# Kernel optimization log

Hardware: AMD Instinct MI355X
Metric: run time of the kernel (lower is better)

## Reference

```python
import jax, jax.numpy as jnp
import numpy as np

N = 65536        # nodes
E = 1048576      # edges (avg degree 16)
G = 512          # graphs
D_IN = 128       # input_dim
D1 = 128         # latent_dim1
D2 = 128         # latent_dim2
L = 3            # layer_num
B = 2            # blocks_num
K = 10           # K_cluster
NF = 16          # num_graph_filter
C = 10           # n_classes
EPS = 1e-5


def setup_inputs():
    key = jax.random.key(0)
    ks = jax.random.split(key, 20)
    s = 0.05
    return {
        "features": jax.random.normal(ks[0], (N, D_IN), jnp.float32),
        "W_row": jax.random.randint(ks[1], (E,), 0, N, jnp.int32),
        "W_col": jax.random.randint(ks[2], (E,), 0, N, jnp.int32),
        "W_vals": jax.random.uniform(ks[3], (E,), jnp.float32),
        "graph_indicator": jnp.sort(jax.random.randint(ks[4], (N,), 0, G, jnp.int32)),
        "targets": jax.random.randint(ks[5], (G,), 0, C, jnp.int32),
        "enc_w1": jax.random.normal(ks[6], (B, D_IN, 2 * D2)) * s,
        "enc_b1": jnp.zeros((B, 2 * D2)),
        "enc_w2": jax.random.normal(ks[7], (B, 2 * D2, D1)) * s,
        "enc_b2": jnp.zeros((B, D1)),
        "bn_gamma": jnp.ones((L + 1, D1)),
        "bn_beta": jnp.zeros((L + 1, D1)),
        "concat_w1": jax.random.normal(ks[8], (L + 1, D2)) * s,
        "concat_b1": jnp.zeros((D2,)),
        "concat_w2": jax.random.normal(ks[9], (D2, 1)) * s,
        "concat_b2": jnp.zeros((1,)),
        "smlp_w1": jax.random.normal(ks[10], (D1, D2)) * s,
        "smlp_b1": jnp.zeros((D2,)),
        "smlp_w2": jax.random.normal(ks[11], (D2, K)) * s,
        "smlp_b2": jnp.zeros((K,)),
        "proto_w1": jax.random.normal(ks[12], (D1, D1)) * s,
        "proto_b1": jnp.zeros((D1,)),
        "proto_w2": jax.random.normal(ks[13], (D1, NF)) * s,
        "proto_b2": jnp.zeros((NF,)),
        "final_w": jax.random.normal(ks[14], (D1 * K, C)) * s,
        "final_b": jnp.zeros((C,)),
        "corr_inter": jax.random.uniform(ks[15], (C, NF)),
        "corr_intra": jax.random.uniform(ks[16], (C, NF)),
    }


def _bn(x, g, b):
    # training-mode batch norm over the node axis (axis=-2), biased variance
    m = x.mean(axis=-2, keepdims=True)
    v = x.var(axis=-2, keepdims=True)
    return (x - m) / jnp.sqrt(v + EPS) * g + b


def reference(features, W_row, W_col, W_vals, graph_indicator, targets,
              enc_w1, enc_b1, enc_w2, enc_b2, bn_gamma, bn_beta,
              concat_w1, concat_b1, concat_w2, concat_b2,
              smlp_w1, smlp_b1, smlp_w2, smlp_b2,
              proto_w1, proto_b1, proto_w2, proto_b2,
              final_w, final_b, corr_inter, corr_intra):
    def spmm(X):  # W @ X via edge list, [N, D] -> [N, D]
        return jax.ops.segment_sum(W_vals[:, None] * X[W_col], W_row, num_segments=N)

    # block encoders -> [B, N, D1]
    h = jax.nn.relu(jnp.einsum('nd,bdh->bnh', features, enc_w1) + enc_b1[:, None, :])
    X_blocks = jnp.einsum('bnh,bho->bno', h, enc_w2) + enc_b2[:, None, :]

    hidden_rep = [X_blocks.mean(0)]
    prop = X_blocks  # holds W^p @ X_b (recursive equivalent of W_list[p] @ X_b)
    for p in range(L):
        prop = jnp.stack([spmm(prop[b]) for b in range(B)])
        Hb = jax.nn.relu(_bn(prop, bn_gamma[p], bn_beta[p]))  # BN per block call, shared params
        hidden_rep.append(Hb.mean(0))

    # concat_mlp acts elementwise per (node, channel) across the layer axis
    Hst = jnp.stack(hidden_rep, axis=-1)  # [N, D1, L+1]
    hc = jax.nn.relu(jnp.einsum('ndl,lh->ndh', Hst, concat_w1) + concat_b1)
    H_all = jnp.einsum('ndh,h->nd', hc, concat_w2[:, 0]) + concat_b2[0]
    H_all = jax.nn.relu(_bn(H_all, bn_gamma[L], bn_beta[L]))

    S_all = jax.nn.softmax(jax.nn.relu(H_all @ smlp_w1 + smlp_b1) @ smlp_w2 + smlp_b2, axis=1)

    # per-graph cluster pooling E_g = S_g^T @ H_g, vectorized via segment_sum
    E_all = jax.ops.segment_sum(S_all[:, :, None] * H_all[:, None, :], graph_indicator, num_segments=G)  # [G, K, D1]

    pred1 = E_all.reshape(G, -1) @ final_w + final_b
    pred_softmax = jax.nn.softmax(pred1, axis=-1)

    sample_cat = jax.random.categorical(jax.random.key(42), pred1, axis=-1)
    ind_positive_sample = sample_cat == targets
    oh = jax.nn.one_hot(sample_cat, C)
    epsilon = jax.lax.stop_gradient(jnp.where(oh != 0, 1.0 - pred_softmax, -pred_softmax))
    sample_cat_oh = pred_softmax + epsilon  # straight-through one-hot

    Q = jax.nn.softmax(jax.nn.relu(E_all @ proto_w1 + proto_b1) @ proto_w2 + proto_b2, axis=-1)  # [G, K, NF]
    corr = jax.nn.softmax(corr_inter, axis=0) * jax.nn.softmax(corr_intra, axis=1)  # [C, NF]
    corr_mask = sample_cat_oh @ corr  # [G, NF]
    feature_mask = jnp.sum(Q * corr_mask[:, None, :], axis=-1)  # [G, K]
    pred2 = (feature_mask[:, :, None] * E_all).reshape(G, -1) @ final_w + final_b

    return pred1, pred2, S_all, H_all, ind_positive_sample, E_all, Q
```

## Files before the change

kernel.cpp:

```cpp
#include <hip/hip_runtime.h>
#include <math.h>

#define NN 65536
#define EE 1048576
#define GG 512
#define D  128

typedef float4 f4;

__global__ __launch_bounds__(256) void k_gemm(const float* __restrict__ A,
    const float* __restrict__ B, const float* __restrict__ bias,
    float* __restrict__ C, int M, int N, int K, int relu)
{
    __shared__ __align__(16) float As[16][132];
    __shared__ __align__(16) float Bs[16][132];
    int tid = threadIdx.x;
    int tx = tid & 15, ty = tid >> 4;
    int row0 = blockIdx.y * 128, col0 = blockIdx.x * 128;
    float acc[8][8];
#pragma unroll
    for (int i = 0; i < 8; ++i)
#pragma unroll
        for (int j = 0; j < 8; ++j) acc[i][j] = 0.f;
    int ar = tid >> 1, ac = (tid & 1) * 8;
    int br = tid >> 4, bc = (tid & 15) * 8;
    const float* aptr = A + (size_t)(row0 + ar) * K + ac;
    const float* bptr = B + (size_t)br * N + col0 + bc;

    f4 pa0 = *(const f4*)(aptr);
    f4 pa1 = *(const f4*)(aptr + 4);
    f4 pb0 = *(const f4*)(bptr);
    f4 pb1 = *(const f4*)(bptr + 4);

    for (int k0 = 0; k0 < K; k0 += 16) {
        As[ac + 0][ar] = pa0.x; As[ac + 1][ar] = pa0.y; As[ac + 2][ar] = pa0.z; As[ac + 3][ar] = pa0.w;
        As[ac + 4][ar] = pa1.x; As[ac + 5][ar] = pa1.y; As[ac + 6][ar] = pa1.z; As[ac + 7][ar] = pa1.w;
        *(f4*)&Bs[br][bc] = pb0; *(f4*)&Bs[br][bc + 4] = pb1;
        __syncthreads();
        if (k0 + 16 < K) {
            pa0 = *(const f4*)(aptr + k0 + 16);
            pa1 = *(const f4*)(aptr + k0 + 16 + 4);
            pb0 = *(const f4*)(bptr + (size_t)(k0 + 16) * N);
            pb1 = *(const f4*)(bptr + (size_t)(k0 + 16) * N + 4);
        }
#pragma unroll
        for (int kk = 0; kk < 16; ++kk) {
            float a[8], b[8];
            *(f4*)&a[0] = *(const f4*)&As[kk][ty * 4];
            *(f4*)&a[4] = *(const f4*)&As[kk][64 + ty * 4];
            *(f4*)&b[0] = *(const f4*)&Bs[kk][tx * 4];
            *(f4*)&b[4] = *(const f4*)&Bs[kk][64 + tx * 4];
#pragma unroll
            for (int i = 0; i < 8; ++i)
#pragma unroll
                for (int j = 0; j < 8; ++j) acc[i][j] = fmaf(a[i], b[j], acc[i][j]);
        }
        __syncthreads();
    }
    f4 bia0 = *(const f4*)(bias + col0 + tx * 4);
    f4 bia1 = *(const f4*)(bias + col0 + 64 + tx * 4);
#pragma unroll
    for (int i = 0; i < 8; ++i) {
        int r = row0 + ((i < 4) ? (ty * 4 + i) : (64 + ty * 4 + i - 4));
        f4 v0, v1;
#pragma unroll
        for (int j = 0; j < 4; ++j) {
            float u0 = acc[i][j] + (&bia0.x)[j];
            float u1 = acc[i][j + 4] + (&bia1.x)[j];
            if (relu) { u0 = fmaxf(u0, 0.f); u1 = fmaxf(u1, 0.f); }
            (&v0.x)[j] = u0; (&v1.x)[j] = u1;
        }
        *(f4*)(C + (size_t)r * N + col0 + tx * 4) = v0;
        *(f4*)(C + (size_t)r * N + col0 + 64 + tx * 4) = v1;
    }
}

__global__ __launch_bounds__(256) void k_hist(const int* __restrict__ Wr, int* __restrict__ cnt)
{
    int e = blockIdx.x * 256 + threadIdx.x;
    if (e < EE) atomicAdd(&cnt[Wr[e]], 1);
}

__global__ __launch_bounds__(256) void k_scan1(const int* __restrict__ cnt,
    int* __restrict__ excl, int* __restrict__ bsum)
{
    __shared__ int s[256];
    int b = blockIdx.x, t = threadIdx.x;
    int v = cnt[b * 256 + t];
    s[t] = v; __syncthreads();
    for (int o = 1; o < 256; o <<= 1) {
        int x = (t >= o) ? s[t - o] : 0;
        __syncthreads();
        s[t] += x;
        __syncthreads();
    }
    excl[b * 256 + t] = s[t] - v;
    if (t == 255) bsum[b] = s[255];
}

__global__ void k_scan2(const int* __restrict__ bsum, int* __restrict__ boff)
{
    __shared__ int s[256];
    int t = threadIdx.x;
    int v = bsum[t]; s[t] = v; __syncthreads();
    for (int o = 1; o < 256; o <<= 1) {
        int x = (t >= o) ? s[t - o] : 0;
        __syncthreads();
        s[t] += x;
        __syncthreads();
    }
    boff[t] = s[t] - v;
}

__global__ __launch_bounds__(256) void k_scan3(const int* __restrict__ excl, const int* __restrict__ boff,
    int* __restrict__ rowptr, int* __restrict__ cursor)
{
    int i = blockIdx.x * 256 + threadIdx.x;
    int v = excl[i] + boff[i >> 8];
    rowptr[i] = v; cursor[i] = v;
    if (i == 0) rowptr[NN] = EE;
}

__global__ __launch_bounds__(256) void k_scatter(const int* __restrict__ Wr, const int* __restrict__ Wc,
    const float* __restrict__ Wv, int* __restrict__ cursor, int* __restrict__ ecol, float* __restrict__ ev)
{
    int e = blockIdx.x * 256 + threadIdx.x;
    if (e >= EE) return;
    int r = Wr[e];
    int p = atomicAdd(&cursor[r], 1);
    ecol[p] = Wc[e]; ev[p] = Wv[e];
}

__global__ __launch_bounds__(256) void k_spmm(const int* __restrict__ rowptr,
    const int* __restrict__ ecol, const float* __restrict__ eval,
    const float* __restrict__ X, float* __restrict__ Y)
{
    int row = blockIdx.x * 4 + (threadIdx.x >> 6);
    int lane = threadIdx.x & 63;
    int s = rowptr[row], e = rowptr[row + 1];
    float a0 = 0.f, a1 = 0.f;
    int i = s;
    for (; i + 4 <= e; i += 4) {
        int   c0 = ecol[i], c1 = ecol[i + 1], c2 = ecol[i + 2], c3 = ecol[i + 3];
        float w0 = eval[i], w1 = eval[i + 1], w2 = eval[i + 2], w3 = eval[i + 3];
        float2 x0 = *(const float2*)(X + (size_t)c0 * D + lane * 2);
        float2 x1 = *(const float2*)(X + (size_t)c1 * D + lane * 2);
        float2 x2 = *(const float2*)(X + (size_t)c2 * D + lane * 2);
        float2 x3 = *(const float2*)(X + (size_t)c3 * D + lane * 2);
        a0 = fmaf(w0, x0.x, a0); a1 = fmaf(w0, x0.y, a1);
        a0 = fmaf(w1, x1.x, a0); a1 = fmaf(w1, x1.y, a1);
        a0 = fmaf(w2, x2.x, a0); a1 = fmaf(w2, x2.y, a1);
        a0 = fmaf(w3, x3.x, a0); a1 = fmaf(w3, x3.y, a1);
    }
    for (; i < e; ++i) {
        int cc = ecol[i];
        float w = eval[i];
        float2 x = *(const float2*)(X + (size_t)cc * D + lane * 2);
        a0 = fmaf(w, x.x, a0);
        a1 = fmaf(w, x.y, a1);
    }
    *(float2*)(Y + (size_t)row * D + lane * 2) = make_float2(a0, a1);
}

__global__ __launch_bounds__(128) void k_bnstats2(const float* __restrict__ X0, const float* __restrict__ X1,
    double* __restrict__ psum, double* __restrict__ pssq)
{
    const float* __restrict__ X = blockIdx.y ? X1 : X0;
    int d = threadIdx.x;
    int r0 = blockIdx.x * 128;
    double s = 0.0, q = 0.0;
#pragma unroll 4
    for (int r = r0; r < r0 + 128; ++r) {
        double v = (double)X[(size_t)r * D + d];
        s += v; q = fma(v, v, q);
    }
    psum[blockIdx.y * 65536 + blockIdx.x * 128 + d] = s;
    pssq[blockIdx.y * 65536 + blockIdx.x * 128 + d] = q;
}

__global__ void k_bnfin(const double* __restrict__ psum, const double* __restrict__ pssq,
    const float* __restrict__ gamma, const float* __restrict__ beta,
    double* __restrict__ a, double* __restrict__ c, int nb, int layer)
{
    int t = threadIdx.x;
    if (t >= nb * 128) return;
    int blk = t >> 7, d = t & 127;
    const double* ps = psum + blk * 65536;
    const double* pq = pssq + blk * 65536;
    double s = 0.0, q = 0.0;
    for (int j = 0; j < 512; ++j) { s += ps[j * 128 + d]; q += pq[j * 128 + d]; }
    double m = s * (1.0 / 65536.0);
    double v = q * (1.0 / 65536.0) - m * m;
    double aa = (double)gamma[layer * 128 + d] / sqrt(v + 1e-5);
    a[t] = aa;
    c[t] = (double)beta[layer * 128 + d] - m * aa;
}

__global__ __launch_bounds__(256) void k_mean2(const f4* __restrict__ x0, const f4* __restrict__ x1,
                                               f4* __restrict__ o)
{
    int i = blockIdx.x * 256 + threadIdx.x;
    f4 a = x0[i], b = x1[i];
    f4 r;
    r.x = 0.5f * (a.x + b.x); r.y = 0.5f * (a.y + b.y);
    r.z = 0.5f * (a.z + b.z); r.w = 0.5f * (a.w + b.w);
    o[i] = r;
}

__global__ __launch_bounds__(256) void k_hidden(const f4* __restrict__ p0, const f4* __restrict__ p1,
    const double* __restrict__ a, const double* __restrict__ c, f4* __restrict__ o)
{
    int i = blockIdx.x * 256 + threadIdx.x;
    int d4 = (i & 31) * 4;
    f4 x = p0[i], y = p1[i];
    f4 r;
#pragma unroll
    for (int j = 0; j < 4; ++j) {
        float a0 = (float)a[d4 + j], c0 = (float)c[d4 + j];
        float a1 = (float)a[128 + d4 + j], c1 = (float)c[128 + d4 + j];
        float xv = (&x.x)[j], yv = (&y.x)[j];
        (&r.x)[j] = 0.5f * (fmaxf(fmaf(xv, a0, c0), 0.f) + fmaxf(fmaf(yv, a1, c1), 0.f));
    }
    o[i] = r;
}

__global__ __launch_bounds__(256) void k_bnapply(f4* __restrict__ H,
    const double* __restrict__ a, const double* __restrict__ c)
{
    int i = blockIdx.x * 256 + threadIdx.x;
    int d4 = (i & 31) * 4;
    f4 x = H[i];
#pragma unroll
    for (int j = 0; j < 4; ++j) {
        float a0 = (float)a[d4 + j], c0 = (float)c[d4 + j];
        (&x.x)[j] = fmaxf(fmaf((&x.x)[j], a0, c0), 0.f);
    }
    H[i] = x;
}

__global__ __launch_bounds__(256) void k_concat(const f4* __restrict__ h0, const f4* __restrict__ h1,
    const f4* __restrict__ h2, const f4* __restrict__ h3,
    const float* __restrict__ w1, const float* __restrict__ b1,
    const float* __restrict__ w2, const float* __restrict__ b2,
    f4* __restrict__ Hpre)
{
    __shared__ __align__(16) float sw0[128], sw1_[128], sw2_[128], sw3[128], sv[128], sb[128];
    int t = threadIdx.x;
    if (t < 128) {
        sw0[t] = w1[t];        sw1_[t] = w1[128 + t];
        sw2_[t] = w1[256 + t]; sw3[t]  = w1[384 + t];
        sv[t]  = w2[t];        sb[t]   = b1[t];
    }
    __syncthreads();
    int i = blockIdx.x * 256 + t;
    f4 x0 = h0[i], x1 = h1[i], x2 = h2[i], x3 = h3[i];
    float bb2 = b2[0];
    float acc0 = bb2, acc1 = bb2, acc2 = bb2, acc3 = bb2;
    for (int h4 = 0; h4 < D; h4 += 4) {
        f4 cw0 = *(const f4*)&sw0[h4];
        f4 cw1 = *(const f4*)&sw1_[h4];
        f4 cw2 = *(const f4*)&sw2_[h4];
        f4 cw3 = *(const f4*)&sw3[h4];
        f4 cbb = *(const f4*)&sb[h4];
        f4 cvv = *(const f4*)&sv[h4];
#pragma unroll
        for (int j = 0; j < 4; ++j) {
            float w0 = (&cw0.x)[j], ww1 = (&cw1.x)[j], ww2 = (&cw2.x)[j], w3 = (&cw3.x)[j];
            float bb = (&cbb.x)[j], vv = (&cvv.x)[j];
            float t0 = fmaf(x3.x, w3, fmaf(x2.x, ww2, fmaf(x1.x, ww1, fmaf(x0.x, w0, bb))));
            float t1 = fmaf(x3.y, w3, fmaf(x2.y, ww2, fmaf(x1.y, ww1, fmaf(x0.y, w0, bb))));
            float t2 = fmaf(x3.z, w3, fmaf(x2.z, ww2, fmaf(x1.z, ww1, fmaf(x0.z, w0, bb))));
            float t3 = fmaf(x3.w, w3, fmaf(x2.w, ww2, fmaf(x1.w, ww1, fmaf(x0.w, w0, bb))));
            acc0 = fmaf(fmaxf(t0, 0.f), vv, acc0);
            acc1 = fmaf(fmaxf(t1, 0.f), vv, acc1);
            acc2 = fmaf(fmaxf(t2, 0.f), vv, acc2);
            acc3 = fmaf(fmaxf(t3, 0.f), vv, acc3);
        }
    }
    f4 r; r.x = acc0; r.y = acc1; r.z = acc2; r.w = acc3;
    Hpre[i] = r;
}

__global__ __launch_bounds__(256) void k_s(const float* __restrict__ hid,
    const float* __restrict__ w2, const float* __restrict__ b2, float* __restrict__ S)
{
    int n = blockIdx.x * 256 + threadIdx.x;
    if (n >= NN) return;
    const float* hr = hid + (size_t)n * D;
    float s[10];
#pragma unroll
    for (int k = 0; k < 10; ++k) s[k] = b2[k];
    for (int h = 0; h < D; h += 4) {
        f4 hv = *(const f4*)(hr + h);
#pragma unroll
        for (int k = 0; k < 10; ++k) {
            s[k] = fmaf(hv.x, w2[(h + 0) * 10 + k], s[k]);
            s[k] = fmaf(hv.y, w2[(h + 1) * 10 + k], s[k]);
            s[k] = fmaf(hv.z, w2[(h + 2) * 10 + k], s[k]);
            s[k] = fmaf(hv.w, w2[(h + 3) * 10 + k], s[k]);
        }
    }
    float m = s[0];
#pragma unroll
    for (int k = 1; k < 10; ++k) m = fmaxf(m, s[k]);
    float e[10], sum = 0.f;
#pragma unroll
    for (int k = 0; k < 10; ++k) { e[k] = expf(s[k] - m); sum += e[k]; }
    float inv = 1.f / sum;
#pragma unroll
    for (int k = 0; k < 10; ++k) S[(size_t)n * 10 + k] = e[k] * inv;
}

__global__ __launch_bounds__(256) void k_eall(const float* __restrict__ S, const float* __restrict__ H,
    const int* __restrict__ off, float* __restrict__ Eo, double* __restrict__ E64)
{
    int g = blockIdx.x;
    int d = threadIdx.x & 127;
    int half = threadIdx.x >> 7;
    double acc[5] = {0.0, 0.0, 0.0, 0.0, 0.0};
    int s0 = off[g], s1 = off[g + 1];
    for (int n = s0; n < s1; ++n) {
        double hv = (double)H[(size_t)n * D + d];
#pragma unroll
        for (int j = 0; j < 5; ++j) acc[j] = fma((double)S[(size_t)n * 10 + half * 5 + j], hv, acc[j]);
    }
#pragma unroll
    for (int j = 0; j < 5; ++j) {
        size_t o = (size_t)g * 1280 + (half * 5 + j) * D + d;
        Eo[o] = (float)acc[j];
        E64[o] = acc[j];
    }
}

__global__ void k_off(const int* __restrict__ gi, int* __restrict__ off)
{
    int g = blockIdx.x * 256 + threadIdx.x;
    if (g > GG) return;
    int lo = 0, hi = NN;
    while (lo < hi) { int mid = (lo + hi) >> 1; if (gi[mid] < g) lo = mid + 1; else hi = mid; }
    off[g] = lo;
}

__global__ void k_corr(const float* __restrict__ ci, const float* __restrict__ ca, float* __restrict__ corr)
{
    int t = threadIdx.x;
    if (t >= 160) return;
    int r = t / 16, c = t % 16;
    double m = -1e300;
    for (int i = 0; i < 10; ++i) m = fmax(m, (double)ci[i * 16 + c]);
    double s = 0.0;
    for (int i = 0; i < 10; ++i) s += exp((double)ci[i * 16 + c] - m);
    double vi = exp((double)ci[r * 16 + c] - m) / s;
    double m2 = -1e300;
    for (int j = 0; j < 16; ++j) m2 = fmax(m2, (double)ca[r * 16 + j]);
    double s2 = 0.0;
    for (int j = 0; j < 16; ++j) s2 += exp((double)ca[r * 16 + j] - m2);
    double va = exp((double)ca[r * 16 + c] - m2) / s2;
    corr[t] = (float)(vi * va);
}

__device__ __forceinline__ unsigned tf_rotl(unsigned x, unsigned n) { return (x << n) | (x >> (32u - n)); }

__global__ void k_gumbel(double* __restrict__ out)
{
    int i = blockIdx.x * 256 + threadIdx.x;
    if (i >= 5120) return;
    unsigned x0 = 0u;
    unsigned x1 = (unsigned)i;
    const unsigned ks0 = 0u, ks1 = 42u;
    const unsigned ks2 = 0x1BD11BDAu ^ ks0 ^ ks1;
    x0 += ks0; x1 += ks1;
#define TF_ROUND(rr) { x0 += x1; x1 = tf_rotl(x1, rr); x1 ^= x0; }
    TF_ROUND(13) TF_ROUND(15) TF_ROUND(26) TF_ROUND(6)
    x0 += ks1; x1 += ks2 + 1u;
    TF_ROUND(17) TF_ROUND(29) TF_ROUND(16) TF_ROUND(24)
    x0 += ks2; x1 += ks0 + 2u;
    TF_ROUND(13) TF_ROUND(15) TF_ROUND(26) TF_ROUND(6)
    x0 += ks0; x1 += ks1 + 3u;
    TF_ROUND(17) TF_ROUND(29) TF_ROUND(16) TF_ROUND(24)
    x0 += ks1; x1 += ks2 + 4u;
    TF_ROUND(13) TF_ROUND(15) TF_ROUND(26) TF_ROUND(6)
    x0 += ks2; x1 += ks0 + 5u;
#undef TF_ROUND
    unsigned bits = x0 ^ x1;
    unsigned fb = (bits >> 9) | 0x3f800000u;
    float f = __uint_as_float(fb) - 1.0f;
    const float tinyf = 1.1754943508222875e-38f;
    float u32v = fmaxf(tinyf, f * (1.0f - tinyf) + tinyf);
    out[i] = -log(-log((double)u32v));
}

__global__ __launch_bounds__(64) void k_pred1(const double* __restrict__ E64, const float* __restrict__ fw,
    const float* __restrict__ fb, const double* __restrict__ gum, const int* __restrict__ tgt,
    const float* __restrict__ corr, float* __restrict__ pred1, float* __restrict__ ind,
    float* __restrict__ cmask)
{
    int g = blockIdx.x;
    int l = threadIdx.x;
    double acc[10];
#pragma unroll
    for (int c = 0; c < 10; ++c) acc[c] = 0.0;
    for (int i = l; i < 1280; i += 64) {
        double e = E64[(size_t)g * 1280 + i];
#pragma unroll
        for (int c = 0; c < 10; ++c) acc[c] = fma(e, (double)fw[i * 10 + c], acc[c]);
    }
#pragma unroll
    for (int c = 0; c < 10; ++c) {
        double v = acc[c];
        for (int o = 32; o > 0; o >>= 1) v += __shfl_down(v, o, 64);
        acc[c] = v;
    }
    if (l == 0) {
        double best = -1e300; int bi = 0;
        for (int c = 0; c < 10; ++c) {
            double p = acc[c] + (double)fb[c];
            pred1[g * 10 + c] = (float)p;
            double y = p + gum[g * 10 + c];
            if (y > best) { best = y; bi = c; }
        }
        ind[g] = (bi == tgt[g]) ? 1.f : 0.f;
        for (int f = 0; f < 16; ++f) cmask[g * 16 + f] = corr[bi * 16 + f];
    }
}

__global__ __launch_bounds__(128) void k_q(const float* __restrict__ Eo, const float* __restrict__ w1,
    const float* __restrict__ b1, const float* __restrict__ w2, const float* __restrict__ b2,
    const float* __restrict__ cmask, float* __restrict__ Q, float* __restrict__ fm)
{
    int gk = blockIdx.x;
    int g = gk / 10;
    int h = threadIdx.x;
    __shared__ float e[128];
    __shared__ float hh[128];
    __shared__ float qv[16];
    __shared__ float pr[16];
    e[h] = Eo[(size_t)gk * D + h];
    __syncthreads();
    float acc = b1[h];
#pragma unroll 8
    for (int d = 0; d < D; ++d) acc = fmaf(e[d], w1[d * D + h], acc);
    hh[h] = fmaxf(acc, 0.f);
    __syncthreads();
    if (h < 16) {
        float s = b2[h];
        for (int d = 0; d < D; ++d) s = fmaf(hh[d], w2[d * 16 + h], s);
        qv[h] = s;
    }
    __syncthreads();
    if (h < 16) {
        float m = qv[0];
        for (int f = 1; f < 16; ++f) m = fmaxf(m, qv[f]);
        pr[h] = expf(qv[h] - m);
    }
    __syncthreads();
    if (h < 16) {
        float s = 0.f;
        for (int f = 0; f < 16; ++f) s += pr[f];
        float q = pr[h] / s;
        Q[(size_t)gk * 16 + h] = q;
        qv[h] = q * cmask[g * 16 + h];
    }
    __syncthreads();
    if (h == 0) {
        float s = 0.f;
        for (int f = 0; f < 16; ++f) s += qv[f];
        fm[gk] = s;
    }
}

__global__ __launch_bounds__(64) void k_pred2(const double* __restrict__ E64, const float* __restrict__ fw,
    const float* __restrict__ fb, const float* __restrict__ fm, float* __restrict__ pred2)
{
    int g = blockIdx.x;
    int l = threadIdx.x;
    double acc[10];
#pragma unroll
    for (int c = 0; c < 10; ++c) acc[c] = 0.0;
    for (int i = l; i < 1280; i += 64) {
        int k = i >> 7;
        double e = E64[(size_t)g * 1280 + i] * (double)fm[g * 10 + k];
#pragma unroll
        for (int c = 0; c < 10; ++c) acc[c] = fma(e, (double)fw[i * 10 + c], acc[c]);
    }
#pragma unroll
    for (int c = 0; c < 10; ++c) {
        double v = acc[c];
        for (int o = 32; o > 0; o >>= 1) v += __shfl_down(v, o, 64);
        acc[c] = v;
    }
    if (l == 0)
        for (int c = 0; c < 10; ++c) pred2[g * 10 + c] = (float)(acc[c] + (double)fb[c]);
}

extern "C" void kernel_launch(void* const* d_in, const int* in_sizes, int n_in,
                              void* d_out, int out_size, void* d_ws, size_t ws_size,
                              hipStream_t stream)
{
    const float* features = (const float*)d_in[0];
    const int*   W_row    = (const int*)d_in[1];
    const int*   W_col    = (const int*)d_in[2];
    const float* W_vals   = (const float*)d_in[3];
    const int*   gi       = (const int*)d_in[4];
    const int*   targets  = (const int*)d_in[5];
    const float* enc_w1   = (const float*)d_in[6];
    const float* enc_b1   = (const float*)d_in[7];
    const float* enc_w2   = (const float*)d_in[8];
    const float* enc_b2   = (const float*)d_in[9];
    const float* bn_gamma = (const float*)d_in[10];
    const float* bn_beta  = (const float*)d_in[11];
    const float* concat_w1= (const float*)d_in[12];
    const float* concat_b1= (const float*)d_in[13];
    const float* concat_w2= (const float*)d_in[14];
    const float* concat_b2= (const float*)d_in[15];
    const float* smlp_w1  = (const float*)d_in[16];
    const float* smlp_b1  = (const float*)d_in[17];
    const float* smlp_w2  = (const float*)d_in[18];
    const float* smlp_b2  = (const float*)d_in[19];
    const float* proto_w1 = (const float*)d_in[20];
    const float* proto_b1 = (const float*)d_in[21];
    const float* proto_w2 = (const float*)d_in[22];
    const float* proto_b2 = (const float*)d_in[23];
    const float* final_w  = (const float*)d_in[24];
    const float* final_b  = (const float*)d_in[25];
    const float* corr_i   = (const float*)d_in[26];
    const float* corr_a   = (const float*)d_in[27];

    float* out = (float*)d_out;
    float* o_pred1 = out + 0;
    float* o_pred2 = out + 5120;
    float* o_S     = out + 10240;
    float* o_H     = out + 665600;
    float* o_ind   = out + 9054208;
    float* o_E     = out + 9054720;
    float* o_Q     = out + 9710080;

    char* base = (char*)d_ws;
    size_t off = 0;
    auto alloc = [&](size_t n) -> char* {
        char* r = base + off;
        off = (off + n + 255) & ~(size_t)255;
        return r;
    };
    int*    d_off   = (int*)alloc(513 * 4);
    double* d_a     = (double*)alloc(256 * 8);
    double* d_c     = (double*)alloc(256 * 8);
    double* d_gum   = (double*)alloc(5120 * 8);
    float*  d_corr  = (float*)alloc(160 * 4);
    float*  d_cmask = (float*)alloc(512 * 16 * 4);
    float*  d_fm    = (float*)alloc(5120 * 4);
    double* psum    = (double*)alloc(2 * 512 * 128 * 8);
    double* pssq    = (double*)alloc(2 * 512 * 128 * 8);
    int*    cnt     = (int*)alloc((size_t)NN * 4);
    int*    excl    = (int*)alloc((size_t)NN * 4);
    int*    bsum    = (int*)alloc(256 * 4);
    int*    boff    = (int*)alloc(256 * 4);
    int*    rowptr  = (int*)alloc((size_t)(NN + 1) * 4);
    int*    cursor  = (int*)alloc((size_t)NN * 4);
    int*    ecol    = (int*)alloc((size_t)EE * 4);
    float*  evalv   = (float*)alloc((size_t)EE * 4);
    double* E64     = (double*)alloc((size_t)GG * 1280 * 8);

    const size_t SZ = (size_t)NN * D * 4;
    float* rot0 = (float*)alloc(SZ);
    float* rot1 = (float*)alloc(SZ);
    float* rot2 = (float*)alloc(SZ);
    float* h0   = (float*)alloc(SZ);
    float* h1   = (float*)alloc(SZ);
    float* h2   = (float*)alloc(SZ);
    float* h3   = (float*)alloc(SZ);
    float* Tenc = h0;
    float* hid2 = rot0;

    k_off   <<<3, 256, 0, stream>>>(gi, d_off);
    k_corr  <<<1, 256, 0, stream>>>(corr_i, corr_a, d_corr);
    k_gumbel<<<20, 256, 0, stream>>>(d_gum);

    hipMemsetAsync(cnt, 0, (size_t)NN * 4, stream);
    k_hist   <<<EE / 256, 256, 0, stream>>>(W_row, cnt);
    k_scan1  <<<256, 256, 0, stream>>>(cnt, excl, bsum);
    k_scan2  <<<1, 256, 0, stream>>>(bsum, boff);
    k_scan3  <<<256, 256, 0, stream>>>(excl, boff, rowptr, cursor);
    k_scatter<<<EE / 256, 256, 0, stream>>>(W_row, W_col, W_vals, cursor, ecol, evalv);

    k_gemm<<<dim3(2, 512), 256, 0, stream>>>(features, enc_w1,             enc_b1,       Tenc, NN, 256, 128, 1);
    k_gemm<<<dim3(1, 512), 256, 0, stream>>>(Tenc,     enc_w2,             enc_b2,       rot0, NN, 128, 256, 0);
    k_gemm<<<dim3(2, 512), 256, 0, stream>>>(features, enc_w1 + 128 * 256, enc_b1 + 256, Tenc, NN, 256, 128, 1);
    k_gemm<<<dim3(1, 512), 256, 0, stream>>>(Tenc,     enc_w2 + 256 * 128, enc_b2 + 128, rot1, NN, 128, 256, 0);
    k_mean2<<<8192, 256, 0, stream>>>((const f4*)rot0, (const f4*)rot1, (f4*)h0);

    float* cur0 = rot0;
    float* cur1 = rot1;
    float* fre  = rot2;
    float* hbuf[4] = { h0, h1, h2, h3 };
    for (int p = 0; p < 3; ++p) {
        k_spmm<<<NN / 4, 256, 0, stream>>>(rowptr, ecol, evalv, cur0, fre);
        k_spmm<<<NN / 4, 256, 0, stream>>>(rowptr, ecol, evalv, cur1, cur0);
        k_bnstats2<<<dim3(512, 2), 128, 0, stream>>>(fre, cur0, psum, pssq);
        k_bnfin<<<1, 256, 0, stream>>>(psum, pssq, bn_gamma, bn_beta, d_a, d_c, 2, p);
        k_hidden<<<8192, 256, 0, stream>>>((const f4*)fre, (const f4*)cur0, d_a, d_c, (f4*)hbuf[1 + p]);
        float* t0 = fre; float* t1 = cur0; float* t2 = cur1;
        cur0 = t0; cur1 = t1; fre = t2;
    }

    k_concat<<<8192, 256, 0, stream>>>((const f4*)h0, (const f4*)h1, (const f4*)h2, (const f4*)h3,
                                       concat_w1, concat_b1, concat_w2, concat_b2, (f4*)o_H);
    k_bnstats2<<<dim3(512, 1), 128, 0, stream>>>(o_H, o_H, psum, pssq);
    k_bnfin<<<1, 256, 0, stream>>>(psum, pssq, bn_gamma, bn_beta, d_a, d_c, 1, 3);
    k_bnapply<<<8192, 256, 0, stream>>>((f4*)o_H, d_a, d_c);

    k_gemm<<<dim3(1, 512), 256, 0, stream>>>(o_H, smlp_w1, smlp_b1, hid2, NN, 128, 128, 1);
    k_s<<<256, 256, 0, stream>>>(hid2, smlp_w2, smlp_b2, o_S);

    k_eall <<<512, 256, 0, stream>>>(o_S, o_H, d_off, o_E, E64);
    k_pred1<<<512, 64, 0, stream>>>(E64, final_w, final_b, d_gum, targets, d_corr,
                                    o_pred1, o_ind, d_cmask);
    k_q    <<<5120, 128, 0, stream>>>(o_E, proto_w1, proto_b1, proto_w2, proto_b2,
                                      d_cmask, o_Q, d_fm);
    k_pred2<<<512, 64, 0, stream>>>(E64, final_w, final_b, d_fm, o_pred2);

    (void)in_sizes; (void)n_in; (void)out_size; (void)ws_size;
}
```

Before: 1.325 ms.

## Double-buffer GEMM smem, fuse mean into GEMM epilogue, batch paired SpMMs

The GEMM kernel now double-buffers its shared-memory tiles, so it needs one barrier per k-step instead of two. The epilogue of the last encoder GEMM can also write the average with a second buffer, which removes the separate mean kernel and one full read/write pass. The two SpMM launches per layer are merged into one launch with a 2D grid, and buffers are reassigned so the branches are not overwritten. The cost is double the shared memory per GEMM block, which may reduce occupancy, plus more complex buffer aliasing.

```diff
diff --git a/kernel.cpp b/kernel.cpp
--- a/kernel.cpp
+++ b/kernel.cpp
@@ -10,10 +10,11 @@
 
 __global__ __launch_bounds__(256) void k_gemm(const float* __restrict__ A,
     const float* __restrict__ B, const float* __restrict__ bias,
-    float* __restrict__ C, int M, int N, int K, int relu)
-{
-    __shared__ __align__(16) float As[16][132];
-    __shared__ __align__(16) float Bs[16][132];
+    float* __restrict__ C, const float* __restrict__ mix_src, float* __restrict__ mix_dst,
+    int M, int N, int K, int relu)
+{
+    __shared__ __align__(16) float As[2][16][132];
+    __shared__ __align__(16) float Bs[2][16][132];
     int tid = threadIdx.x;
     int tx = tid & 15, ty = tid >> 4;
     int row0 = blockIdx.y * 128, col0 = blockIdx.x * 128;
@@ -31,32 +32,44 @@
     f4 pa1 = *(const f4*)(aptr + 4);
     f4 pb0 = *(const f4*)(bptr);
     f4 pb1 = *(const f4*)(bptr + 4);
-
+    As[0][ac + 0][ar] = pa0.x; As[0][ac + 1][ar] = pa0.y; As[0][ac + 2][ar] = pa0.z; As[0][ac + 3][ar] = pa0.w;
+    As[0][ac + 4][ar] = pa1.x; As[0][ac + 5][ar] = pa1.y; As[0][ac + 6][ar] = pa1.z; As[0][ac + 7][ar] = pa1.w;
+    *(f4*)&Bs[0][br][bc] = pb0; *(f4*)&Bs[0][br][bc + 4] = pb1;
+    __syncthreads();
+
+    int cur = 0;
     for (int k0 = 0; k0 < K; k0 += 16) {
-        As[ac + 0][ar] = pa0.x; As[ac + 1][ar] = pa0.y; As[ac + 2][ar] = pa0.z; As[ac + 3][ar] = pa0.w;
-        As[ac + 4][ar] = pa1.x; As[ac + 5][ar] = pa1.y; As[ac + 6][ar] = pa1.z; As[ac + 7][ar] = pa1.w;
-        *(f4*)&Bs[br][bc] = pb0; *(f4*)&Bs[br][bc + 4] = pb1;
-        __syncthreads();
-        if (k0 + 16 < K) {
+        int last = (k0 + 16 >= K);
+        if (!last) {
             pa0 = *(const f4*)(aptr + k0 + 16);
             pa1 = *(const f4*)(aptr + k0 + 16 + 4);
             pb0 = *(const f4*)(bptr + (size_t)(k0 + 16) * N);
             pb1 = *(const f4*)(bptr + (size_t)(k0 + 16) * N + 4);
         }
+        const float (*Ac)[132] = As[cur];
+        const float (*Bc)[132] = Bs[cur];
 #pragma unroll
         for (int kk = 0; kk < 16; ++kk) {
             float a[8], b[8];
-            *(f4*)&a[0] = *(const f4*)&As[kk][ty * 4];
-            *(f4*)&a[4] = *(const f4*)&As[kk][64 + ty * 4];
-            *(f4*)&b[0] = *(const f4*)&Bs[kk][tx * 4];
-            *(f4*)&b[4] = *(const f4*)&Bs[kk][64 + tx * 4];
+            *(f4*)&a[0] = *(const f4*)&Ac[kk][ty * 4];
+            *(f4*)&a[4] = *(const f4*)&Ac[kk][64 + ty * 4];
+            *(f4*)&b[0] = *(const f4*)&Bc[kk][tx * 4];
+            *(f4*)&b[4] = *(const f4*)&Bc[kk][64 + tx * 4];
 #pragma unroll
             for (int i = 0; i < 8; ++i)
 #pragma unroll
                 for (int j = 0; j < 8; ++j) acc[i][j] = fmaf(a[i], b[j], acc[i][j]);
         }
-        __syncthreads();
-    }
+        if (!last) {
+            int nxt = cur ^ 1;
+            As[nxt][ac + 0][ar] = pa0.x; As[nxt][ac + 1][ar] = pa0.y; As[nxt][ac + 2][ar] = pa0.z; As[nxt][ac + 3][ar] = pa0.w;
+            As[nxt][ac + 4][ar] = pa1.x; As[nxt][ac + 5][ar] = pa1.y; As[nxt][ac + 6][ar] = pa1.z; As[nxt][ac + 7][ar] = pa1.w;
+            *(f4*)&Bs[nxt][br][bc] = pb0; *(f4*)&Bs[nxt][br][bc + 4] = pb1;
+            __syncthreads();
+            cur = nxt;
+        }
+    }
+
     f4 bia0 = *(const f4*)(bias + col0 + tx * 4);
     f4 bia1 = *(const f4*)(bias + col0 + 64 + tx * 4);
 #pragma unroll
@@ -72,6 +85,18 @@
         }
         *(f4*)(C + (size_t)r * N + col0 + tx * 4) = v0;
         *(f4*)(C + (size_t)r * N + col0 + 64 + tx * 4) = v1;
+        if (mix_dst) {
+            f4 m0 = *(const f4*)(mix_src + (size_t)r * N + col0 + tx * 4);
+            f4 m1 = *(const f4*)(mix_src + (size_t)r * N + col0 + 64 + tx * 4);
+            f4 w0, w1;
+#pragma unroll
+            for (int j = 0; j < 4; ++j) {
+                (&w0.x)[j] = 0.5f * ((&v0.x)[j] + (&m0.x)[j]);
+                (&w1.x)[j] = 0.5f * ((&v1.x)[j] + (&m1.x)[j]);
+            }
+            *(f4*)(mix_dst + (size_t)r * N + col0 + tx * 4) = w0;
+            *(f4*)(mix_dst + (size_t)r * N + col0 + 64 + tx * 4) = w1;
+        }
     }
 }
 
@@ -131,12 +156,15 @@
     ecol[p] = Wc[e]; ev[p] = Wv[e];
 }
 
-__global__ __launch_bounds__(256) void k_spmm(const int* __restrict__ rowptr,
+__global__ __launch_bounds__(256) void k_spmm2(const int* __restrict__ rowptr,
     const int* __restrict__ ecol, const float* __restrict__ eval,
-    const float* __restrict__ X, float* __restrict__ Y)
+    const float* __restrict__ X0, float* __restrict__ Y0,
+    const float* __restrict__ X1, float* __restrict__ Y1)
 {
     int row = blockIdx.x * 4 + (threadIdx.x >> 6);
     int lane = threadIdx.x & 63;
+    const float* __restrict__ X = blockIdx.y ? X1 : X0;
+    float* __restrict__ Y = blockIdx.y ? Y1 : Y0;
     int s = rowptr[row], e = rowptr[row + 1];
     float a0 = 0.f, a1 = 0.f;
     int i = s;
@@ -196,19 +224,8 @@
     c[t] = (double)beta[layer * 128 + d] - m * aa;
 }
 
-__global__ __launch_bounds__(256) void k_mean2(const f4* __restrict__ x0, const f4* __restrict__ x1,
-                                               f4* __restrict__ o)
-{
-    int i = blockIdx.x * 256 + threadIdx.x;
-    f4 a = x0[i], b = x1[i];
-    f4 r;
-    r.x = 0.5f * (a.x + b.x); r.y = 0.5f * (a.y + b.y);
-    r.z = 0.5f * (a.z + b.z); r.w = 0.5f * (a.w + b.w);
-    o[i] = r;
-}
-
-__global__ __launch_bounds__(256) void k_hidden(const f4* __restrict__ p0, const f4* __restrict__ p1,
-    const double* __restrict__ a, const double* __restrict__ c, f4* __restrict__ o)
+__global__ __launch_bounds__(256) void k_hidden(const f4* __restrict__ p0, const f4* p1,
+    const double* __restrict__ a, const double* __restrict__ c, f4* o)
 {
     int i = blockIdx.x * 256 + threadIdx.x;
     int d4 = (i & 31) * 4;
@@ -569,7 +586,7 @@
     float* h1   = (float*)alloc(SZ);
     float* h2   = (float*)alloc(SZ);
     float* h3   = (float*)alloc(SZ);
-    float* Tenc = h0;
+    float* Tenc = h2;
     float* hid2 = rot0;
 
     k_off   <<<3, 256, 0, stream>>>(gi, d_off);
@@ -583,24 +600,25 @@
     k_scan3  <<<256, 256, 0, stream>>>(excl, boff, rowptr, cursor);
     k_scatter<<<EE / 256, 256, 0, stream>>>(W_row, W_col, W_vals, cursor, ecol, evalv);
 
-    k_gemm<<<dim3(2, 512), 256, 0, stream>>>(features, enc_w1,             enc_b1,       Tenc, NN, 256, 128, 1);
-    k_gemm<<<dim3(1, 512), 256, 0, stream>>>(Tenc,     enc_w2,             enc_b2,       rot0, NN, 128, 256, 0);
-    k_gemm<<<dim3(2, 512), 256, 0, stream>>>(features, enc_w1 + 128 * 256, enc_b1 + 256, Tenc, NN, 256, 128, 1);
-    k_gemm<<<dim3(1, 512), 256, 0, stream>>>(Tenc,     enc_w2 + 256 * 128, enc_b2 + 128, rot1, NN, 128, 256, 0);
-    k_mean2<<<8192, 256, 0, stream>>>((const f4*)rot0, (const f4*)rot1, (f4*)h0);
-
-    float* cur0 = rot0;
-    float* cur1 = rot1;
-    float* fre  = rot2;
-    float* hbuf[4] = { h0, h1, h2, h3 };
-    for (int p = 0; p < 3; ++p) {
-        k_spmm<<<NN / 4, 256, 0, stream>>>(rowptr, ecol, evalv, cur0, fre);
-        k_spmm<<<NN / 4, 256, 0, stream>>>(rowptr, ecol, evalv, cur1, cur0);
-        k_bnstats2<<<dim3(512, 2), 128, 0, stream>>>(fre, cur0, psum, pssq);
-        k_bnfin<<<1, 256, 0, stream>>>(psum, pssq, bn_gamma, bn_beta, d_a, d_c, 2, p);
-        k_hidden<<<8192, 256, 0, stream>>>((const f4*)fre, (const f4*)cur0, d_a, d_c, (f4*)hbuf[1 + p]);
-        float* t0 = fre; float* t1 = cur0; float* t2 = cur1;
-        cur0 = t0; cur1 = t1; fre = t2;
+    k_gemm<<<dim3(2, 512), 256, 0, stream>>>(features, enc_w1,             enc_b1,       Tenc, nullptr, nullptr, NN, 256, 128, 1);
+    k_gemm<<<dim3(1, 512), 256, 0, stream>>>(Tenc,     enc_w2,             enc_b2,       rot0, nullptr, nullptr, NN, 128, 256, 0);
+    k_gemm<<<dim3(2, 512), 256, 0, stream>>>(features, enc_w1 + 128 * 256, enc_b1 + 256, Tenc, nullptr, nullptr, NN, 256, 128, 1);
+    k_gemm<<<dim3(1, 512), 256, 0, stream>>>(Tenc,     enc_w2 + 256 * 128, enc_b2 + 128, rot1, rot0, h0,         NN, 128, 256, 0);
+
+    {
+        float* hbuf[4] = { h0, h1, h2, h3 };
+        float* curA = rot0; float* curB = rot1;
+        float* nxtA[3] = { rot2, rot0, rot2 };
+        float* nxtB[3] = { h2,   rot1, h3   };
+        for (int p = 0; p < 3; ++p) {
+            float* nA = nxtA[p];
+            float* nB = nxtB[p];
+            k_spmm2<<<dim3(NN / 4, 2), 256, 0, stream>>>(rowptr, ecol, evalv, curA, nA, curB, nB);
+            k_bnstats2<<<dim3(512, 2), 128, 0, stream>>>(nA, nB, psum, pssq);
+            k_bnfin<<<1, 256, 0, stream>>>(psum, pssq, bn_gamma, bn_beta, d_a, d_c, 2, p);
+            k_hidden<<<8192, 256, 0, stream>>>((const f4*)nA, (const f4*)nB, d_a, d_c, (f4*)hbuf[1 + p]);
+            curA = nA; curB = nB;
+        }
     }
 
     k_concat<<<8192, 256, 0, stream>>>((const f4*)h0, (const f4*)h1, (const f4*)h2, (const f4*)h3,
@@ -609,7 +627,7 @@
     k_bnfin<<<1, 256, 0, stream>>>(psum, pssq, bn_gamma, bn_beta, d_a, d_c, 1, 3);
     k_bnapply<<<8192, 256, 0, stream>>>((f4*)o_H, d_a, d_c);
 
-    k_gemm<<<dim3(1, 512), 256, 0, stream>>>(o_H, smlp_w1, smlp_b1, hid2, NN, 128, 128, 1);
+    k_gemm<<<dim3(1, 512), 256, 0, stream>>>(o_H, smlp_w1, smlp_b1, hid2, nullptr, nullptr, NN, 128, 128, 1);
     k_s<<<256, 256, 0, stream>>>(hid2, smlp_w2, smlp_b2, o_S);
 
     k_eall <<<512, 256, 0, stream>>>(o_S, o_H, d_off, o_E, E64);
```

Measured after the change: 1.310 ms, median of 2. Within noise of the previous version (-1.1%).
